# Performance work log

Measured on AMD Instinct MI355X. Metric: run time of the kernel, lower is better.

## Reference

```python
import jax, jax.numpy as jnp
import numpy as np

S, T, N, D, H, DT = 4, 4, 65536, 128, 128, 128


def setup_inputs() -> dict:
    key = jax.random.key(0)
    ks = jax.random.split(key, 9)
    inv_d = 1.0 / np.sqrt(D)
    inv_h = 1.0 / np.sqrt(H)
    return {
        "states": jax.random.normal(ks[0], (N, D), dtype=jnp.float32),
        "scores": jax.random.uniform(ks[1], (N, 1), dtype=jnp.float32),
        "type_ids": jax.random.randint(ks[2], (N,), 0, S, dtype=jnp.int32),
        "type_matching": jax.random.normal(ks[3], (S, T), dtype=jnp.float32),
        "W1": jax.random.normal(ks[4], (S, T, D, H), dtype=jnp.float32) * inv_d,
        "b1": jnp.zeros((S, T, H), dtype=jnp.float32),
        "W2": jax.random.normal(ks[5], (S, T, H, DT), dtype=jnp.float32) * inv_h,
        "b2": jnp.zeros((S, T, DT), dtype=jnp.float32),
        "C1": jax.random.normal(ks[6], (S, T, D, H), dtype=jnp.float32) * inv_d,
        "c1": jnp.zeros((S, T, H), dtype=jnp.float32),
        "C2": jax.random.normal(ks[7], (S, T, H, 1), dtype=jnp.float32) * inv_h,
        "c2": jnp.zeros((S, T, 1), dtype=jnp.float32),
    }


def reference(states, scores, type_ids, type_matching, W1, b1, W2, b2, C1, c1, C2, c2):
    """Batched MetaphorMorphism.forward with best_match_only=True.

    For each item with source type s: route to t* = argmax sigmoid(type_matching[s]),
    apply mapper MLP (D->H->DT, ReLU), classifier MLP (D->H->1, ReLU, sigmoid),
    new_score = min(score, classifier_out), item_prob = sigmoid(type_matching)[s, t*].
    """
    match_sig = jax.nn.sigmoid(type_matching)          # [S, T]
    best_t = jnp.argmax(type_matching, axis=1)         # [S] (argmax of sigmoid == argmax of logits)
    best_prob = match_sig[jnp.arange(S), best_t]       # [S]

    out_state = jnp.zeros((states.shape[0], W2.shape[-1]), dtype=states.dtype)
    out_score = jnp.zeros_like(scores)
    # loop over the small, fixed set of source types (structurally distinct experts)
    for s in range(S):
        t = best_t[s]
        h = jax.nn.relu(states @ W1[s, t] + b1[s, t])          # [N, H]
        y = h @ W2[s, t] + b2[s, t]                            # [N, DT]
        hc = jax.nn.relu(states @ C1[s, t] + c1[s, t])         # [N, H]
        cls = jax.nn.sigmoid(hc @ C2[s, t] + c2[s, t])         # [N, 1]
        new_score = jnp.minimum(scores, cls)                   # [N, 1]
        m = (type_ids == s)[:, None]
        out_state = jnp.where(m, y, out_state)
        out_score = jnp.where(m, new_score, out_score)
    item_prob = best_prob[type_ids]                            # [N]
    return out_state, out_score, item_prob
```

## Files before the change

### kernel.cpp

```cpp
#include <hip/hip_runtime.h>
#include <math.h>

#define Nn 65536

typedef short s16x8 __attribute__((ext_vector_type(8)));
typedef float f32x4 __attribute__((ext_vector_type(4)));
typedef unsigned int u32;

__device__ __forceinline__ unsigned short f2bf(float x) {
    u32 u = __float_as_uint(x);
    u += 0x7FFFu + ((u >> 16) & 1u);
    return (unsigned short)(u >> 16);
}

__device__ __forceinline__ int best_t_for(const float* __restrict__ tm, int s, float* mOut) {
    float m = tm[s * 4];
    int am = 0;
#pragma unroll
    for (int j = 1; j < 4; ++j) {
        float v = tm[s * 4 + j];
        if (v > m) { m = v; am = j; }
    }
    if (mOut) *mOut = m;
    return am;
}

__global__ void k_prepw(const float* __restrict__ tm,
                        const float* __restrict__ W1, const float* __restrict__ W2,
                        const float* __restrict__ C1, unsigned short* __restrict__ wbf) {
    int u = blockIdx.x * 256 + threadIdx.x;
    int mat = u >> 11;
    int rr = u & 2047;
    int f = rr >> 6, lane = rr & 63;
    int kk = f >> 3, n8 = f & 7;
    int q = lane >> 4, l15 = lane & 15;
    int sm = mat / 3, w = mat - sm * 3;
    int t = best_t_for(tm, sm, nullptr);
    const float* src = (w == 0) ? W1 : (w == 1) ? W2 : C1;
    const float* sp = src + (((sm * 4 + t) << 14) + n8 * 16 + l15);
    int k0 = kk * 32 + q * 8;
    s16x8 o;
#pragma unroll
    for (int j = 0; j < 8; ++j) o[j] = (short)f2bf(sp[(k0 + j) * 128]);
    *(s16x8*)(wbf + (size_t)u * 8) = o;
}

__global__ __launch_bounds__(512, 4) void k_fused(
    const float* __restrict__ states, const float* __restrict__ scores,
    const int* __restrict__ type_ids, const float* __restrict__ tm,
    const float* __restrict__ b1g, const float* __restrict__ b2g,
    const float* __restrict__ c1g, const float* __restrict__ C2,
    const float* __restrict__ c2, const unsigned short* __restrict__ wbf,
    float* __restrict__ out_state, float* __restrict__ out_score,
    float* __restrict__ out_prob)
{
    __shared__ __align__(16) unsigned short Abuf[128 * 128];
    __shared__ __align__(16) unsigned short Hbuf[176 * 128];
    __shared__ int permLds[176];
    __shared__ float pSum[176];
    __shared__ int wcnt[2][4];

    const int t = threadIdx.x;
    const int gid0 = blockIdx.x * 128;
    const int lane = t & 63;
    const int wv = t >> 6;
    const int l15 = lane & 15;
    const int quad = lane >> 4;
    const int myRow = t >> 2;
    const int q4 = t & 3;
    const int col = wv * 16 + l15;

    int stIdx4[4];
    float bmax[4];
#pragma unroll
    for (int s = 0; s < 4; ++s) stIdx4[s] = s * 4 + best_t_for(tm, s, &bmax[s]);

    if (t < 176) { permLds[t] = -1; pSum[t] = 0.f; }

    {
        const int g = gid0 + myRow;
        const float4* sp = (const float4*)(states + (size_t)g * 128 + q4 * 32);
        float4 v[8];
#pragma unroll
        for (int i = 0; i < 8; ++i) v[i] = sp[i];
        unsigned short* dstRow = &Abuf[myRow * 128];
        const int rot = (myRow & 15) << 3;
#pragma unroll
        for (int i = 0; i < 8; ++i) {
            int c = (q4 * 32 + i * 4 + rot) & 127;
            ushort4 o;
            o.x = f2bf(v[i].x); o.y = f2bf(v[i].y);
            o.z = f2bf(v[i].z); o.w = f2bf(v[i].w);
            *(ushort4*)(dstRow + c) = o;
        }
    }

    int myty = 0, w2 = 0;
    unsigned long long msk = 0;
    if (t < 128) {
        w2 = t >> 6;
        myty = type_ids[gid0 + t];
#pragma unroll
        for (int sv = 0; sv < 4; ++sv) {
            unsigned long long mm = __ballot(myty == sv);
            if (myty == sv) msk = mm;
            if (lane == 0) wcnt[w2][sv] = (int)__popcll(mm);
        }
    }
    __syncthreads();

    int nsA[4], sbA[4], G;
    {
        int sb = 0;
#pragma unroll
        for (int sv = 0; sv < 4; ++sv) {
            int c = wcnt[0][sv] + wcnt[1][sv];
            nsA[sv] = (c + 15) >> 4;
            sbA[sv] = sb;
            sb += nsA[sv];
        }
        G = sb;
    }
    if (t < 128) {
        unsigned long long lt = (1ull << lane) - 1ull;
        int pos = sbA[myty] * 16 + ((w2 == 1) ? wcnt[0][myty] : 0) + (int)__popcll(msk & lt);
        permLds[pos] = t;
    }
    __syncthreads();

    const unsigned short* __restrict__ wbase = wbf;
    s16x8 wf[4];
    auto loadWf = [&](int ty, int m) {
        const unsigned short* wb = wbase + ((size_t)ty * 3 + m) * 16384;
#pragma unroll
        for (int kk = 0; kk < 4; ++kk)
            wf[kk] = *(const s16x8*)(wb + (size_t)((kk * 8 + wv) * 64 + lane) * 8);
    };
    auto gemmA = [&](int seg) -> f32x4 {
        f32x4 acc = {0.f, 0.f, 0.f, 0.f};
        int pRow = permLds[seg * 16 + l15];
        int rr = (pRow >= 0) ? pRow : 0;
        const int rbase = rr * 128;
        const int rot = (rr & 15) << 3;
#pragma unroll
        for (int kk = 0; kk < 4; ++kk) {
            s16x8 af = *(const s16x8*)(Abuf + rbase + ((kk * 32 + quad * 8 + rot) & 127));
            acc = __builtin_amdgcn_mfma_f32_16x16x32_bf16(af, wf[kk], acc, 0, 0, 0);
        }
        return acc;
    };
    auto gemmH = [&](int seg) -> f32x4 {
        f32x4 acc = {0.f, 0.f, 0.f, 0.f};
        const unsigned short* hb = Hbuf + (seg * 16 + l15) * 128;
#pragma unroll
        for (int kk = 0; kk < 4; ++kk) {
            s16x8 af = *(const s16x8*)(hb + ((kk * 32 + quad * 8 + (l15 << 3)) & 127));
            acc = __builtin_amdgcn_mfma_f32_16x16x32_bf16(af, wf[kk], acc, 0, 0, 0);
        }
        return acc;
    };

    for (int ty = 0; ty < 4; ++ty) {
        const int ns = nsA[ty];
        if (ns == 0) continue;
        const int sb = sbA[ty];
        const int si0 = stIdx4[ty];

        loadWf(ty, 0);
        {
            const float b1v = b1g[si0 * 128 + col];
            for (int si = 0; si < ns; ++si) {
                const int seg = sb + si;
                f32x4 a = gemmA(seg);
#pragma unroll
                for (int r = 0; r < 4; ++r) {
                    int row = seg * 16 + quad * 4 + r;
                    float v = fmaxf(a[r] + b1v, 0.f);
                    Hbuf[row * 128 + ((col + ((row & 15) << 3)) & 127)] = f2bf(v);
                }
            }
        }
        __syncthreads();

        loadWf(ty, 1);
        {
            const float b2v = b2g[si0 * 128 + col];
            for (int si = 0; si < ns; ++si) {
                const int seg = sb + si;
                f32x4 a = gemmH(seg);
#pragma unroll
                for (int r = 0; r < 4; ++r) {
                    int p = permLds[seg * 16 + quad * 4 + r];
                    if (p >= 0) out_state[(size_t)(gid0 + p) * 128 + col] = a[r] + b2v;
                }
            }
        }

        loadWf(ty, 2);
        {
            const float c1v = c1g[si0 * 128 + col];
            const float c2w = C2[si0 * 128 + col];
            for (int si = 0; si < ns; ++si) {
                const int seg = sb + si;
                f32x4 a = gemmA(seg);
                float part[4];
#pragma unroll
                for (int r = 0; r < 4; ++r) part[r] = fmaxf(a[r] + c1v, 0.f) * c2w;
#pragma unroll
                for (int off = 1; off < 16; off <<= 1)
#pragma unroll
                    for (int r = 0; r < 4; ++r)
                        part[r] += __shfl_xor(part[r], off, 64);
                if (l15 == 0) {
#pragma unroll
                    for (int r = 0; r < 4; ++r)
                        atomicAdd(&pSum[seg * 16 + quad * 4 + r], part[r]);
                }
            }
        }
    }
    __syncthreads();

    if (t < G * 16) {
        int p = permLds[t];
        if (p >= 0) {
            int seg = t >> 4;
            int sty = (seg >= sbA[1] ? 1 : 0) + (seg >= sbA[2] ? 1 : 0) + (seg >= sbA[3] ? 1 : 0);
            float tot = pSum[t] + c2[stIdx4[sty]];
            float cls = 1.f / (1.f + expf(-tot));
            out_score[gid0 + p] = fminf(scores[gid0 + p], cls);
            out_prob[gid0 + p] = 1.f / (1.f + expf(-bmax[sty]));
        }
    }
}

extern "C" void kernel_launch(void* const* d_in, const int* in_sizes, int n_in,
                              void* d_out, int out_size, void* d_ws, size_t ws_size,
                              hipStream_t stream) {
    const float* states = (const float*)d_in[0];
    const float* scores = (const float*)d_in[1];
    const int*   type_ids = (const int*)d_in[2];
    const float* tm = (const float*)d_in[3];
    const float* W1 = (const float*)d_in[4];
    const float* b1 = (const float*)d_in[5];
    const float* W2 = (const float*)d_in[6];
    const float* b2 = (const float*)d_in[7];
    const float* C1 = (const float*)d_in[8];
    const float* c1 = (const float*)d_in[9];
    const float* C2 = (const float*)d_in[10];
    const float* c2 = (const float*)d_in[11];

    unsigned short* wbf = (unsigned short*)d_ws;

    float* out_state = (float*)d_out;
    float* out_score = out_state + (size_t)Nn * 128;
    float* out_prob  = out_score + Nn;

    k_prepw<<<96, 256, 0, stream>>>(tm, W1, W2, C1, wbf);
    k_fused<<<512, 512, 0, stream>>>(states, scores, type_ids, tm, b1, b2, c1,
        C2, c2, wbf, out_state, out_score, out_prob);
}
```

Measured before the change: 128.6 us.

## Fuse W1 and C1 GEMMs sharing A-fragment loads and batch per-type barriers

```diff
diff --git a/kernel.cpp b/kernel.cpp
--- a/kernel.cpp
+++ b/kernel.cpp
@@ -54,9 +54,10 @@
     float* __restrict__ out_state, float* __restrict__ out_score,
     float* __restrict__ out_prob)
 {
-    __shared__ __align__(16) unsigned short Abuf[128 * 128];
+    __shared__ __align__(16) unsigned short Abuf[129 * 128];
     __shared__ __align__(16) unsigned short Hbuf[176 * 128];
     __shared__ int permLds[176];
+    __shared__ int islotLds[128];
     __shared__ float pSum[176];
     __shared__ int wcnt[2][4];
 
@@ -76,15 +77,50 @@
     for (int s = 0; s < 4; ++s) stIdx4[s] = s * 4 + best_t_for(tm, s, &bmax[s]);
 
     if (t < 176) { permLds[t] = -1; pSum[t] = 0.f; }
-
+    if (t >= 256 && t < 272)
+        ((int4*)(Abuf + 128 * 128))[t - 256] = int4{0, 0, 0, 0};
+
+    int myty = 0, w2 = 0;
+    unsigned long long msk = 0;
+    if (t < 128) {
+        w2 = t >> 6;
+        myty = type_ids[gid0 + t];
+#pragma unroll
+        for (int sv = 0; sv < 4; ++sv) {
+            unsigned long long mm = __ballot(myty == sv);
+            if (myty == sv) msk = mm;
+            if (lane == 0) wcnt[w2][sv] = (int)__popcll(mm);
+        }
+    }
+    __syncthreads();
+
+    int nsA[4], sbA[4], G;
     {
-        const int g = gid0 + myRow;
-        const float4* sp = (const float4*)(states + (size_t)g * 128 + q4 * 32);
+        int sb = 0;
+#pragma unroll
+        for (int sv = 0; sv < 4; ++sv) {
+            int c = wcnt[0][sv] + wcnt[1][sv];
+            nsA[sv] = (c + 15) >> 4;
+            sbA[sv] = sb;
+            sb += nsA[sv];
+        }
+        G = sb;
+    }
+    if (t < 128) {
+        unsigned long long lt = (1ull << lane) - 1ull;
+        int pos = sbA[myty] * 16 + ((w2 == 1) ? wcnt[0][myty] : 0) + (int)__popcll(msk & lt);
+        permLds[pos] = t;
+        islotLds[t] = pos;
+    }
+    __syncthreads();
+
+    {
+        const int rot = (islotLds[myRow] & 15) << 3;
+        const float4* sp = (const float4*)(states + (size_t)(gid0 + myRow) * 128 + q4 * 32);
         float4 v[8];
 #pragma unroll
         for (int i = 0; i < 8; ++i) v[i] = sp[i];
         unsigned short* dstRow = &Abuf[myRow * 128];
-        const int rot = (myRow & 15) << 3;
 #pragma unroll
         for (int i = 0; i < 8; ++i) {
             int c = (q4 * 32 + i * 4 + rot) & 127;
@@ -94,70 +130,15 @@
             *(ushort4*)(dstRow + c) = o;
         }
     }
-
-    int myty = 0, w2 = 0;
-    unsigned long long msk = 0;
-    if (t < 128) {
-        w2 = t >> 6;
-        myty = type_ids[gid0 + t];
-#pragma unroll
-        for (int sv = 0; sv < 4; ++sv) {
-            unsigned long long mm = __ballot(myty == sv);
-            if (myty == sv) msk = mm;
-            if (lane == 0) wcnt[w2][sv] = (int)__popcll(mm);
-        }
-    }
-    __syncthreads();
-
-    int nsA[4], sbA[4], G;
-    {
-        int sb = 0;
-#pragma unroll
-        for (int sv = 0; sv < 4; ++sv) {
-            int c = wcnt[0][sv] + wcnt[1][sv];
-            nsA[sv] = (c + 15) >> 4;
-            sbA[sv] = sb;
-            sb += nsA[sv];
-        }
-        G = sb;
-    }
-    if (t < 128) {
-        unsigned long long lt = (1ull << lane) - 1ull;
-        int pos = sbA[myty] * 16 + ((w2 == 1) ? wcnt[0][myty] : 0) + (int)__popcll(msk & lt);
-        permLds[pos] = t;
-    }
     __syncthreads();
 
     const unsigned short* __restrict__ wbase = wbf;
-    s16x8 wf[4];
-    auto loadWf = [&](int ty, int m) {
+    s16x8 wfA[4], wfC[4];
+    auto loadWf = [&](int ty, int m, s16x8 wf[4]) {
         const unsigned short* wb = wbase + ((size_t)ty * 3 + m) * 16384;
 #pragma unroll
         for (int kk = 0; kk < 4; ++kk)
             wf[kk] = *(const s16x8*)(wb + (size_t)((kk * 8 + wv) * 64 + lane) * 8);
-    };
-    auto gemmA = [&](int seg) -> f32x4 {
-        f32x4 acc = {0.f, 0.f, 0.f, 0.f};
-        int pRow = permLds[seg * 16 + l15];
-        int rr = (pRow >= 0) ? pRow : 0;
-        const int rbase = rr * 128;
-        const int rot = (rr & 15) << 3;
-#pragma unroll
-        for (int kk = 0; kk < 4; ++kk) {
-            s16x8 af = *(const s16x8*)(Abuf + rbase + ((kk * 32 + quad * 8 + rot) & 127));
-            acc = __builtin_amdgcn_mfma_f32_16x16x32_bf16(af, wf[kk], acc, 0, 0, 0);
-        }
-        return acc;
-    };
-    auto gemmH = [&](int seg) -> f32x4 {
-        f32x4 acc = {0.f, 0.f, 0.f, 0.f};
-        const unsigned short* hb = Hbuf + (seg * 16 + l15) * 128;
-#pragma unroll
-        for (int kk = 0; kk < 4; ++kk) {
-            s16x8 af = *(const s16x8*)(hb + ((kk * 32 + quad * 8 + (l15 << 3)) & 127));
-            acc = __builtin_amdgcn_mfma_f32_16x16x32_bf16(af, wf[kk], acc, 0, 0, 0);
-        }
-        return acc;
     };
 
     for (int ty = 0; ty < 4; ++ty) {
@@ -165,61 +146,69 @@
         if (ns == 0) continue;
         const int sb = sbA[ty];
         const int si0 = stIdx4[ty];
-
-        loadWf(ty, 0);
-        {
-            const float b1v = b1g[si0 * 128 + col];
-            for (int si = 0; si < ns; ++si) {
-                const int seg = sb + si;
-                f32x4 a = gemmA(seg);
-#pragma unroll
-                for (int r = 0; r < 4; ++r) {
-                    int row = seg * 16 + quad * 4 + r;
-                    float v = fmaxf(a[r] + b1v, 0.f);
-                    Hbuf[row * 128 + ((col + ((row & 15) << 3)) & 127)] = f2bf(v);
-                }
-            }
-        }
-        __syncthreads();
-
-        loadWf(ty, 1);
-        {
-            const float b2v = b2g[si0 * 128 + col];
-            for (int si = 0; si < ns; ++si) {
-                const int seg = sb + si;
-                f32x4 a = gemmH(seg);
-#pragma unroll
-                for (int r = 0; r < 4; ++r) {
-                    int p = permLds[seg * 16 + quad * 4 + r];
-                    if (p >= 0) out_state[(size_t)(gid0 + p) * 128 + col] = a[r] + b2v;
-                }
-            }
-        }
-
-        loadWf(ty, 2);
-        {
-            const float c1v = c1g[si0 * 128 + col];
-            const float c2w = C2[si0 * 128 + col];
-            for (int si = 0; si < ns; ++si) {
-                const int seg = sb + si;
-                f32x4 a = gemmA(seg);
-                float part[4];
-#pragma unroll
-                for (int r = 0; r < 4; ++r) part[r] = fmaxf(a[r] + c1v, 0.f) * c2w;
-#pragma unroll
-                for (int off = 1; off < 16; off <<= 1)
-#pragma unroll
-                    for (int r = 0; r < 4; ++r)
-                        part[r] += __shfl_xor(part[r], off, 64);
-                if (l15 == 0) {
-#pragma unroll
-                    for (int r = 0; r < 4; ++r)
-                        atomicAdd(&pSum[seg * 16 + quad * 4 + r], part[r]);
-                }
-            }
-        }
-    }
-    __syncthreads();
+        loadWf(ty, 0, wfA);
+        loadWf(ty, 2, wfC);
+        const float b1v = b1g[si0 * 128 + col];
+        const float c1v = c1g[si0 * 128 + col];
+        const float c2w = C2[si0 * 128 + col];
+        for (int si = 0; si < ns; ++si) {
+            const int seg = sb + si;
+            int pRow = permLds[seg * 16 + l15];
+            const unsigned short* ab = Abuf + ((pRow >= 0) ? pRow : 128) * 128;
+            const int rotc = l15 << 3;
+            f32x4 a1 = {0.f, 0.f, 0.f, 0.f};
+            f32x4 a3 = {0.f, 0.f, 0.f, 0.f};
+#pragma unroll
+            for (int kk = 0; kk < 4; ++kk) {
+                s16x8 af = *(const s16x8*)(ab + ((kk * 32 + quad * 8 + rotc) & 127));
+                a1 = __builtin_amdgcn_mfma_f32_16x16x32_bf16(af, wfA[kk], a1, 0, 0, 0);
+                a3 = __builtin_amdgcn_mfma_f32_16x16x32_bf16(af, wfC[kk], a3, 0, 0, 0);
+            }
+#pragma unroll
+            for (int r = 0; r < 4; ++r) {
+                int row = seg * 16 + quad * 4 + r;
+                float v = fmaxf(a1[r] + b1v, 0.f);
+                Hbuf[row * 128 + ((col + ((row & 15) << 3)) & 127)] = f2bf(v);
+            }
+            float part[4];
+#pragma unroll
+            for (int r = 0; r < 4; ++r) part[r] = fmaxf(a3[r] + c1v, 0.f) * c2w;
+#pragma unroll
+            for (int off = 1; off < 16; off <<= 1)
+#pragma unroll
+                for (int r = 0; r < 4; ++r) part[r] += __shfl_xor(part[r], off, 64);
+            if (l15 == 0) {
+#pragma unroll
+                for (int r = 0; r < 4; ++r)
+                    atomicAdd(&pSum[seg * 16 + quad * 4 + r], part[r]);
+            }
+        }
+    }
+    __syncthreads();
+
+    for (int ty = 0; ty < 4; ++ty) {
+        const int ns = nsA[ty];
+        if (ns == 0) continue;
+        const int sb = sbA[ty];
+        const int si0 = stIdx4[ty];
+        loadWf(ty, 1, wfA);
+        const float b2v = b2g[si0 * 128 + col];
+        for (int si = 0; si < ns; ++si) {
+            const int seg = sb + si;
+            const unsigned short* hb = Hbuf + (seg * 16 + l15) * 128;
+            f32x4 a = {0.f, 0.f, 0.f, 0.f};
+#pragma unroll
+            for (int kk = 0; kk < 4; ++kk) {
+                s16x8 af = *(const s16x8*)(hb + ((kk * 32 + quad * 8 + (l15 << 3)) & 127));
+                a = __builtin_amdgcn_mfma_f32_16x16x32_bf16(af, wfA[kk], a, 0, 0, 0);
+            }
+#pragma unroll
+            for (int r = 0; r < 4; ++r) {
+                int p = permLds[seg * 16 + quad * 4 + r];
+                if (p >= 0) out_state[(size_t)(gid0 + p) * 128 + col] = a[r] + b2v;
+            }
+        }
+    }
 
     if (t < G * 16) {
         int p = permLds[t];
```

Measured after the change: 128.6 us. Within noise of the previous version (+0.0%).

## Halve rows per block, shrink LDS, reuse per-type H buffer for higher occupancy

Applied to the files above, without the earlier changes.

```diff
diff --git a/kernel.cpp b/kernel.cpp
--- a/kernel.cpp
+++ b/kernel.cpp
@@ -45,7 +45,7 @@
     *(s16x8*)(wbf + (size_t)u * 8) = o;
 }
 
-__global__ __launch_bounds__(512, 4) void k_fused(
+__global__ __launch_bounds__(512, 8) void k_fused(
     const float* __restrict__ states, const float* __restrict__ scores,
     const int* __restrict__ type_ids, const float* __restrict__ tm,
     const float* __restrict__ b1g, const float* __restrict__ b2g,
@@ -54,40 +54,44 @@
     float* __restrict__ out_state, float* __restrict__ out_score,
     float* __restrict__ out_prob)
 {
-    __shared__ __align__(16) unsigned short Abuf[128 * 128];
-    __shared__ __align__(16) unsigned short Hbuf[176 * 128];
-    __shared__ int permLds[176];
-    __shared__ float pSum[176];
-    __shared__ int wcnt[2][4];
+    __shared__ __align__(16) unsigned short Abuf[65 * 128];
+    __shared__ __align__(16) unsigned short Hbuf[64 * 128];
+    __shared__ int permLds[112];
+    __shared__ float pSum[112];
+    __shared__ float scoreLds[64];
+    __shared__ int wcnt[4];
 
     const int t = threadIdx.x;
-    const int gid0 = blockIdx.x * 128;
+    const int gid0 = blockIdx.x * 64;
     const int lane = t & 63;
     const int wv = t >> 6;
     const int l15 = lane & 15;
     const int quad = lane >> 4;
-    const int myRow = t >> 2;
-    const int q4 = t & 3;
+    const int myRow = t >> 3;
+    const int q8 = t & 7;
     const int col = wv * 16 + l15;
 
     int stIdx4[4];
     float bmax[4];
 #pragma unroll
     for (int s = 0; s < 4; ++s) stIdx4[s] = s * 4 + best_t_for(tm, s, &bmax[s]);
-
-    if (t < 176) { permLds[t] = -1; pSum[t] = 0.f; }
+    float c2v0 = c2[stIdx4[0]], c2v1 = c2[stIdx4[1]];
+    float c2v2 = c2[stIdx4[2]], c2v3 = c2[stIdx4[3]];
+
+    if (t < 112) { permLds[t] = -1; pSum[t] = 0.f; }
+    if (t >= 448 && t < 464)
+        ((int4*)(Abuf + 64 * 128))[t - 448] = int4{0, 0, 0, 0};
 
     {
-        const int g = gid0 + myRow;
-        const float4* sp = (const float4*)(states + (size_t)g * 128 + q4 * 32);
-        float4 v[8];
-#pragma unroll
-        for (int i = 0; i < 8; ++i) v[i] = sp[i];
+        const float4* sp = (const float4*)(states + (size_t)(gid0 + myRow) * 128 + q8 * 16);
+        float4 v[4];
+#pragma unroll
+        for (int i = 0; i < 4; ++i) v[i] = sp[i];
         unsigned short* dstRow = &Abuf[myRow * 128];
         const int rot = (myRow & 15) << 3;
 #pragma unroll
-        for (int i = 0; i < 8; ++i) {
-            int c = (q4 * 32 + i * 4 + rot) & 127;
+        for (int i = 0; i < 4; ++i) {
+            int c = (q8 * 16 + i * 4 + rot) & 127;
             ushort4 o;
             o.x = f2bf(v[i].x); o.y = f2bf(v[i].y);
             o.z = f2bf(v[i].z); o.w = f2bf(v[i].w);
@@ -95,17 +99,26 @@
         }
     }
 
-    int myty = 0, w2 = 0;
-    unsigned long long msk = 0;
-    if (t < 128) {
-        w2 = t >> 6;
-        myty = type_ids[gid0 + t];
-#pragma unroll
-        for (int sv = 0; sv < 4; ++sv) {
-            unsigned long long mm = __ballot(myty == sv);
-            if (myty == sv) msk = mm;
-            if (lane == 0) wcnt[w2][sv] = (int)__popcll(mm);
-        }
+    if (t < 64) {
+        int myty = type_ids[gid0 + t];
+        scoreLds[t] = scores[gid0 + t];
+        unsigned long long msk = 0;
+        int c0 = 0, c1 = 0, c2_ = 0, c3 = 0;
+        {
+            unsigned long long m0 = __ballot(myty == 0);
+            unsigned long long m1 = __ballot(myty == 1);
+            unsigned long long m2 = __ballot(myty == 2);
+            unsigned long long m3 = __ballot(myty == 3);
+            msk = (myty == 0) ? m0 : (myty == 1) ? m1 : (myty == 2) ? m2 : m3;
+            c0 = (int)__popcll(m0); c1 = (int)__popcll(m1);
+            c2_ = (int)__popcll(m2); c3 = (int)__popcll(m3);
+        }
+        if (t == 0) { wcnt[0] = c0; wcnt[1] = c1; wcnt[2] = c2_; wcnt[3] = c3; }
+        int ns0 = (c0 + 15) >> 4, ns1 = (c1 + 15) >> 4, ns2 = (c2_ + 15) >> 4;
+        int sb1 = ns0, sb2 = ns0 + ns1, sb3 = ns0 + ns1 + ns2;
+        int sbMy = (myty == 0) ? 0 : (myty == 1) ? sb1 : (myty == 2) ? sb2 : sb3;
+        unsigned long long lt = (1ull << t) - 1ull;
+        permLds[sbMy * 16 + (int)__popcll(msk & lt)] = t;
     }
     __syncthreads();
 
@@ -114,19 +127,12 @@
         int sb = 0;
 #pragma unroll
         for (int sv = 0; sv < 4; ++sv) {
-            int c = wcnt[0][sv] + wcnt[1][sv];
-            nsA[sv] = (c + 15) >> 4;
+            nsA[sv] = (wcnt[sv] + 15) >> 4;
             sbA[sv] = sb;
             sb += nsA[sv];
         }
         G = sb;
     }
-    if (t < 128) {
-        unsigned long long lt = (1ull << lane) - 1ull;
-        int pos = sbA[myty] * 16 + ((w2 == 1) ? wcnt[0][myty] : 0) + (int)__popcll(msk & lt);
-        permLds[pos] = t;
-    }
-    __syncthreads();
 
     const unsigned short* __restrict__ wbase = wbf;
     s16x8 wf[4];
@@ -139,19 +145,19 @@
     auto gemmA = [&](int seg) -> f32x4 {
         f32x4 acc = {0.f, 0.f, 0.f, 0.f};
         int pRow = permLds[seg * 16 + l15];
-        int rr = (pRow >= 0) ? pRow : 0;
-        const int rbase = rr * 128;
+        int rr = (pRow >= 0) ? pRow : 64;
+        const unsigned short* ab = Abuf + rr * 128;
         const int rot = (rr & 15) << 3;
 #pragma unroll
         for (int kk = 0; kk < 4; ++kk) {
-            s16x8 af = *(const s16x8*)(Abuf + rbase + ((kk * 32 + quad * 8 + rot) & 127));
+            s16x8 af = *(const s16x8*)(ab + ((kk * 32 + quad * 8 + rot) & 127));
             acc = __builtin_amdgcn_mfma_f32_16x16x32_bf16(af, wf[kk], acc, 0, 0, 0);
         }
         return acc;
     };
-    auto gemmH = [&](int seg) -> f32x4 {
+    auto gemmH = [&](int si) -> f32x4 {
         f32x4 acc = {0.f, 0.f, 0.f, 0.f};
-        const unsigned short* hb = Hbuf + (seg * 16 + l15) * 128;
+        const unsigned short* hb = Hbuf + (si * 16 + l15) * 128;
 #pragma unroll
         for (int kk = 0; kk < 4; ++kk) {
             s16x8 af = *(const s16x8*)(hb + ((kk * 32 + quad * 8 + (l15 << 3)) & 127));
@@ -160,6 +166,7 @@
         return acc;
     };
 
+#pragma unroll
     for (int ty = 0; ty < 4; ++ty) {
         const int ns = nsA[ty];
         if (ns == 0) continue;
@@ -170,32 +177,15 @@
         {
             const float b1v = b1g[si0 * 128 + col];
             for (int si = 0; si < ns; ++si) {
-                const int seg = sb + si;
-                f32x4 a = gemmA(seg);
+                f32x4 a = gemmA(sb + si);
 #pragma unroll
                 for (int r = 0; r < 4; ++r) {
-                    int row = seg * 16 + quad * 4 + r;
+                    int row = si * 16 + quad * 4 + r;
                     float v = fmaxf(a[r] + b1v, 0.f);
                     Hbuf[row * 128 + ((col + ((row & 15) << 3)) & 127)] = f2bf(v);
                 }
             }
         }
-        __syncthreads();
-
-        loadWf(ty, 1);
-        {
-            const float b2v = b2g[si0 * 128 + col];
-            for (int si = 0; si < ns; ++si) {
-                const int seg = sb + si;
-                f32x4 a = gemmH(seg);
-#pragma unroll
-                for (int r = 0; r < 4; ++r) {
-                    int p = permLds[seg * 16 + quad * 4 + r];
-                    if (p >= 0) out_state[(size_t)(gid0 + p) * 128 + col] = a[r] + b2v;
-                }
-            }
-        }
-
         loadWf(ty, 2);
         {
             const float c1v = c1g[si0 * 128 + col];
@@ -209,8 +199,7 @@
 #pragma unroll
                 for (int off = 1; off < 16; off <<= 1)
 #pragma unroll
-                    for (int r = 0; r < 4; ++r)
-                        part[r] += __shfl_xor(part[r], off, 64);
+                    for (int r = 0; r < 4; ++r) part[r] += __shfl_xor(part[r], off, 64);
                 if (l15 == 0) {
 #pragma unroll
                     for (int r = 0; r < 4; ++r)
@@ -218,18 +207,34 @@
                 }
             }
         }
-    }
-    __syncthreads();
+        __syncthreads();
+
+        loadWf(ty, 1);
+        {
+            const float b2v = b2g[si0 * 128 + col];
+            for (int si = 0; si < ns; ++si) {
+                f32x4 a = gemmH(si);
+#pragma unroll
+                for (int r = 0; r < 4; ++r) {
+                    int p = permLds[(sb + si) * 16 + quad * 4 + r];
+                    if (p >= 0) out_state[(size_t)(gid0 + p) * 128 + col] = a[r] + b2v;
+                }
+            }
+        }
+        __syncthreads();
+    }
 
     if (t < G * 16) {
         int p = permLds[t];
         if (p >= 0) {
             int seg = t >> 4;
             int sty = (seg >= sbA[1] ? 1 : 0) + (seg >= sbA[2] ? 1 : 0) + (seg >= sbA[3] ? 1 : 0);
-            float tot = pSum[t] + c2[stIdx4[sty]];
+            float c2s = (sty == 0) ? c2v0 : (sty == 1) ? c2v1 : (sty == 2) ? c2v2 : c2v3;
+            float bm = (sty == 0) ? bmax[0] : (sty == 1) ? bmax[1] : (sty == 2) ? bmax[2] : bmax[3];
+            float tot = pSum[t] + c2s;
             float cls = 1.f / (1.f + expf(-tot));
-            out_score[gid0 + p] = fminf(scores[gid0 + p], cls);
-            out_prob[gid0 + p] = 1.f / (1.f + expf(-bmax[sty]));
+            out_score[gid0 + p] = fminf(scoreLds[p], cls);
+            out_prob[gid0 + p] = 1.f / (1.f + expf(-bm));
         }
     }
 }
@@ -257,6 +262,6 @@
     float* out_prob  = out_score + Nn;
 
     k_prepw<<<96, 256, 0, stream>>>(tm, W1, W2, C1, wbf);
-    k_fused<<<512, 512, 0, stream>>>(states, scores, type_ids, tm, b1, b2, c1,
+    k_fused<<<1024, 512, 0, stream>>>(states, scores, type_ids, tm, b1, b2, c1,
         C2, c2, wbf, out_state, out_score, out_prob);
 }
```

Measured after the change: 131.8 us. 1.02x slower.
